# Kernel tuning notes

Measured on AMD Instinct MI355X. Metric: run time of the kernel, lower is better.

The kernel has to match this reference:

```python
import jax, jax.numpy as jnp
import numpy as np

BETA = 0.25
N_E = 8192
E_DIM = 256


def setup_inputs() -> dict:
    key = jax.random.key(0)
    k1, k2 = jax.random.split(key)
    z = jax.random.normal(k1, (16, E_DIM, 32, 32), dtype=jnp.float32)
    # matches torch init: uniform_(-1/n_e, 1/n_e)
    codebook = jax.random.uniform(k2, (N_E, E_DIM), dtype=jnp.float32,
                                  minval=-1.0 / N_E, maxval=1.0 / N_E)
    return {"z": z, "codebook": codebook}


def reference(z, codebook):
    B, C, H, W = z.shape  # C == e_dim
    zp = jnp.transpose(z, (0, 2, 3, 1))          # [B, H, W, C]
    zf = zp.reshape(-1, C)                       # [N, C], N = B*H*W
    # squared L2 distances: ||z||^2 + ||e||^2 - 2 z.e
    d = (jnp.sum(zf * zf, axis=1, keepdims=True)
         + jnp.sum(codebook * codebook, axis=1)
         - 2.0 * jnp.einsum('nc,kc->nk', zf, codebook))  # [N, n_e]
    min_encoding_indices = jnp.argmin(d, axis=1)         # [N]
    z_q = codebook[min_encoding_indices].reshape(zp.shape)  # [B, H, W, C]
    sg = jax.lax.stop_gradient
    loss = jnp.mean((sg(z_q) - zp) ** 2) + BETA * jnp.mean((z_q - sg(zp)) ** 2)
    # straight-through estimator
    z_q_st = zp + sg(z_q - zp)
    z_q_out = jnp.transpose(z_q_st, (0, 3, 1, 2))  # back to NCHW
    return z_q_out, loss, min_encoding_indices
```

## Files before the change

kernel.cpp:

```cpp
#include <hip/hip_runtime.h>

typedef short s8v __attribute__((ext_vector_type(8)));
typedef float f4v __attribute__((ext_vector_type(4)));
typedef float f4 __attribute__((ext_vector_type(4)));
typedef unsigned short u16v4 __attribute__((ext_vector_type(4)));

#define N_PIX 16384
#define NE    8192
#define EDIM  256
#define ZQ_ELEMS 4194304
#define MARGIN 4.5e-4f
#define NGRP 512

__device__ __forceinline__ float bf2f(unsigned short u) {
    union { unsigned int i; float f; } c; c.i = ((unsigned int)u) << 16; return c.f;
}
__device__ __forceinline__ unsigned short f2bf(float f) {
    unsigned int u = __float_as_uint(f);
    u = (u + 0x7fffu + ((u >> 16) & 1u)) >> 16;
    return (unsigned short)u;
}
__device__ __forceinline__ unsigned short f2bf_down(float f) {
    unsigned int u = __float_as_uint(f);
    unsigned short b = (unsigned short)(u >> 16);
    if ((u & 0xFFFFu) && (u >> 31)) b += 1;
    return b;
}

__device__ __forceinline__ float np_pw128sq(const float* a) {
    float r[8];
    #pragma unroll
    for (int j = 0; j < 8; ++j) r[j] = __fmul_rn(a[j], a[j]);
    for (int i = 8; i < 128; i += 8)
        #pragma unroll
        for (int j = 0; j < 8; ++j) r[j] = __fadd_rn(r[j], __fmul_rn(a[i + j], a[i + j]));
    return __fadd_rn(__fadd_rn(__fadd_rn(r[0], r[1]), __fadd_rn(r[2], r[3])),
                     __fadd_rn(__fadd_rn(r[4], r[5]), __fadd_rn(r[6], r[7])));
}


__global__ __launch_bounds__(256) void vq_pre(const float* __restrict__ z,
                                              const float* __restrict__ cb,
                                              unsigned short* __restrict__ z16,
                                              unsigned short* __restrict__ cb16,
                                              float* __restrict__ esum32,
                                              int do_z) {
    __shared__ unsigned short zl[64 * 66];
    int t = threadIdx.x;
    int bx = blockIdx.x;
    if (bx < 1024) {
        if (!do_z) return;
        int p0 = (bx >> 2) * 64;
        int c0 = (bx & 3) * 64;
        int b = p0 >> 10, hw0 = p0 & 1023;
        const float* src = z + (((size_t)b * 256 + c0) << 10) + hw0;
        #pragma unroll
        for (int i = 0; i < 4; ++i) {
            int idx = i * 256 + t;
            int ch = idx >> 4, pq = idx & 15;
            f4 v = *(const f4*)(src + ((size_t)ch << 10) + pq * 4);
            #pragma unroll
            for (int e = 0; e < 4; ++e) zl[(pq * 4 + e) * 66 + ch] = f2bf(v[e]);
        }
        __syncthreads();
        #pragma unroll
        for (int i = 0; i < 2; ++i) {
            int idx = i * 256 + t;
            int px = idx >> 3, cc = idx & 7;
            s8v o;
            #pragma unroll
            for (int e = 0; e < 8; ++e) o[e] = (short)zl[px * 66 + cc * 8 + e];
            *(s8v*)&z16[((size_t)(p0 + px)) * 256 + c0 + cc * 8] = o;
        }
    } else {
        int base = (bx - 1024) * 32;
        const float* src = cb + (size_t)base * EDIM;
        unsigned short* dst = cb16 + (size_t)base * EDIM;
        #pragma unroll
        for (int i = 0; i < 8; ++i) {
            int e0 = (i * 256 + t) * 4;
            f4 v = *(const f4*)(src + e0);
            u16v4 o;
            o.x = f2bf(v[0]); o.y = f2bf(v[1]); o.z = f2bf(v[2]); o.w = f2bf(v[3]);
            *(u16v4*)(dst + e0) = o;
        }
        if (t < 32) {
            const float* a = cb + (size_t)(base + t) * EDIM;
            esum32[base + t] = __fadd_rn(np_pw128sq(a), np_pw128sq(a + 128));
        }
    }
}

__global__ __launch_bounds__(512, 2) void vq_phase1g(const unsigned short* __restrict__ cb16,
                                                     const unsigned short* __restrict__ z16,
                                                     unsigned short* __restrict__ gmin) {
    __shared__ unsigned short L[2][32768];
    const int t = threadIdx.x;
    const int wave = t >> 6, lane = t & 63;
    const int q = lane >> 4, r = lane & 15;
    const int wr = wave >> 2, wc = wave & 3;
    const int cm0 = ((int)blockIdx.x >> 3) * 256;
    const int pg  = (int)blockIdx.x & 7;

    const int pc0 = t, pc1 = t + 512;
    const int row0 = pc0 >> 2, row1 = pc1 >> 2;
    const int lc0 = (pc0 & 3) ^ ((row0 >> 1) & 3);
    const int lc1 = (pc1 & 3) ^ ((row1 >> 1) & 3);
    const int go0 = row0 * 256 + lc0 * 8;
    const int go1 = row1 * 256 + lc1 * 8;
    const int ld0 = pc0 * 8;
    const int ld1 = pc1 * 8;

    const unsigned short* gA = cb16 + (size_t)cm0 * 256;
    const unsigned short* gB0 = z16 + (size_t)pg * 2048 * 256;

    f4v acc[8][4];
    const f4v zz = {0.f, 0.f, 0.f, 0.f};
    #pragma unroll
    for (int mi = 0; mi < 8; ++mi)
        #pragma unroll
        for (int ni = 0; ni < 4; ++ni) acc[mi][ni] = zz;

    const int cxo = (q ^ ((r >> 1) & 3)) * 8;
    const int aro = (wr * 128 + r) * 32 + cxo;
    const int bro = 16384 + (wc * 64 + r) * 32 + cxo;

#define GLL(g, l) __builtin_amdgcn_global_load_lds( \
        (const __attribute__((address_space(1))) unsigned int*)(g), \
        (__attribute__((address_space(3))) unsigned int*)(l), 16, 0, 0)
#define STAGEKT(buf_, gk_, gBp_) do { \
        unsigned short* Lb_ = &L[(buf_)][0]; \
        GLL(gA + go0 + (gk_),            Lb_ + ld0); \
        GLL(gA + go1 + (gk_),            Lb_ + ld1); \
        GLL(gA + go0 + 32 + (gk_),       Lb_ + 8192 + ld0); \
        GLL(gA + go1 + 32 + (gk_),       Lb_ + 8192 + ld1); \
        GLL((gBp_) + go0 + (gk_),        Lb_ + 16384 + ld0); \
        GLL((gBp_) + go1 + (gk_),        Lb_ + 16384 + ld1); \
        GLL((gBp_) + go0 + 32 + (gk_),   Lb_ + 16384 + 8192 + ld0); \
        GLL((gBp_) + go1 + 32 + (gk_),   Lb_ + 16384 + 8192 + ld1); } while (0)
#define ARD(Lp, mi, ks) (*(const s8v*)&(Lp)[(ks) * 8192 + (mi) * 512 + aro])
#define BRD(Lp, ni, ks) (*(const s8v*)&(Lp)[(ks) * 8192 + (ni) * 512 + bro])
#define MFMA16(Aset, Bset, mo) do { \
        __builtin_amdgcn_s_setprio(1); \
        _Pragma("unroll") \
        for (int mi = 0; mi < 4; ++mi) \
            _Pragma("unroll") \
            for (int ni = 0; ni < 4; ++ni) \
                acc[(mo) + mi][ni] = __builtin_amdgcn_mfma_f32_16x16x32_bf16( \
                    Aset[mi], Bset[ni], acc[(mo) + mi][ni], 0, 0, 0); \
        __builtin_amdgcn_s_setprio(0); } while (0)

    STAGEKT(0, 0, gB0);
    asm volatile("s_waitcnt vmcnt(0)" ::: "memory");
    __builtin_amdgcn_s_barrier();

    for (int it = 0; it < 32; ++it) {
        const int buf = it & 1;
        const unsigned short* Lb = &L[buf][0];
        const int nit = it + 1;
        const bool st = nit < 32;

        __builtin_amdgcn_s_barrier();
        if (st) {
            STAGEKT(buf ^ 1, (nit & 3) * 64, gB0 + (size_t)(nit >> 2) * 65536);
            asm volatile("s_waitcnt vmcnt(8)" ::: "memory");
        } else {
            asm volatile("s_waitcnt vmcnt(0)" ::: "memory");
        }
        __builtin_amdgcn_s_barrier();
        __builtin_amdgcn_sched_barrier(0);

        s8v A0[4], A1[4], B0[4], B1[4];
        #pragma unroll
        for (int ni = 0; ni < 4; ++ni) B0[ni] = BRD(Lb, ni, 0);
        #pragma unroll
        for (int mi = 0; mi < 4; ++mi) A0[mi] = ARD(Lb, mi, 0);
        #pragma unroll
        for (int mi = 0; mi < 4; ++mi) A1[mi] = ARD(Lb, 4 + mi, 0);
        __builtin_amdgcn_sched_barrier(0);
        MFMA16(A0, B0, 0);

        #pragma unroll
        for (int mi = 0; mi < 4; ++mi) A0[mi] = ARD(Lb, mi, 1);
        #pragma unroll
        for (int ni = 0; ni < 4; ++ni) B1[ni] = BRD(Lb, ni, 1);
        __builtin_amdgcn_sched_barrier(0);
        MFMA16(A1, B0, 4);

        #pragma unroll
        for (int mi = 0; mi < 4; ++mi) A1[mi] = ARD(Lb, 4 + mi, 1);
        __builtin_amdgcn_sched_barrier(0);
        MFMA16(A0, B1, 0);

        __builtin_amdgcn_sched_barrier(0);
        MFMA16(A1, B1, 4);

        if ((it & 3) == 3) {
            const int pn0 = pg * 2048 + (it >> 2) * 256;
            #pragma unroll
            for (int mi = 0; mi < 8; ++mi) {
                int g = cm0 / 16 + wr * 8 + mi;
                #pragma unroll
                for (int ni = 0; ni < 4; ++ni) {
                    f4v a = acc[mi][ni];
                    float mx = fmaxf(fmaxf(a[0], a[1]), fmaxf(a[2], a[3]));
                    mx = fmaxf(mx, __shfl_xor(mx, 16));
                    mx = fmaxf(mx, __shfl_xor(mx, 32));
                    if (q == 0) {
                        int pxc = (pn0 + wc * 64 + ni * 16) >> 4;
                        gmin[(size_t)pxc * 8192 + g * 16 + r] = f2bf_down(-2.0f * mx);
                    }
                    acc[mi][ni] = zz;
                }
            }
        }
    }
#undef MFMA16
#undef BRD
#undef ARD
#undef STAGEKT
#undef GLL
}

__global__ __launch_bounds__(512, 2) void vq_phase1(const float* __restrict__ z,
                                                    const unsigned short* __restrict__ cb16,
                                                    unsigned short* __restrict__ gmin) {
    const int t = threadIdx.x;
    const int wave = t >> 6, lane = t & 63;
    const int col = lane & 15, q = lane >> 4;
    const int mb = (blockIdx.x >> 1) * 64;
    const int chalf = blockIdx.x & 1;

    s8v Z[4][8];
    #pragma unroll
    for (int pt = 0; pt < 4; ++pt) {
        int n = mb + pt * 16 + col;
        const float* zb = z + ((size_t)(n >> 10) << 18) + (size_t)(n & 1023);
        #pragma unroll
        for (int c0 = 0; c0 < 8; ++c0) {
            s8v a;
            #pragma unroll
            for (int j = 0; j < 8; ++j) {
                int c = c0 * 32 + q * 8 + j;
                a[j] = (short)f2bf(zb[(size_t)c << 10]);
            }
            Z[pt][c0] = a;
        }
    }

    const int kbase = chalf * 4096 + wave * 512;
    for (int it = 0; it < 16; ++it) {
        int n0 = kbase + it * 32;
        const unsigned short* bb = cb16 + (size_t)(n0 + col) * EDIM + q * 8;
        f4v zz = {0.f, 0.f, 0.f, 0.f};
        f4v acc[4][2];
        #pragma unroll
        for (int pt = 0; pt < 4; ++pt) { acc[pt][0] = zz; acc[pt][1] = zz; }
        #pragma unroll
        for (int c0 = 0; c0 < 8; ++c0) {
            s8v C0 = *(const s8v*)(bb + c0 * 32);
            s8v C1 = *(const s8v*)(bb + 16 * EDIM + c0 * 32);
            #pragma unroll
            for (int pt = 0; pt < 4; ++pt) {
                acc[pt][0] = __builtin_amdgcn_mfma_f32_16x16x32_bf16(C0, Z[pt][c0], acc[pt][0], 0, 0, 0);
                acc[pt][1] = __builtin_amdgcn_mfma_f32_16x16x32_bf16(C1, Z[pt][c0], acc[pt][1], 0, 0, 0);
            }
        }
        int gbase = chalf * 256 + wave * 32 + it * 2;
        #pragma unroll
        for (int pt = 0; pt < 4; ++pt) {
            #pragma unroll
            for (int s = 0; s < 2; ++s) {
                f4v a = acc[pt][s];
                float mx = fmaxf(fmaxf(a[0], a[1]), fmaxf(a[2], a[3]));
                mx = fmaxf(mx, __shfl_xor(mx, 16));
                mx = fmaxf(mx, __shfl_xor(mx, 32));
                if (q == 0)
                    gmin[(size_t)((mb >> 4) + pt) * 8192 + (gbase + s) * 16 + col] =
                        f2bf_down(-2.0f * mx);
            }
        }
    }
}

__global__ __launch_bounds__(256) void vq_phase2(const float* __restrict__ z,
                                                 const float* __restrict__ cb,
                                                 const float* __restrict__ esum32,
                                                 const unsigned short* __restrict__ gmin,
                                                 unsigned int* __restrict__ idxw) {
    __shared__ float zt[32 * 260];
    __shared__ unsigned short gm[NGRP * 33];
    __shared__ float zs[32];
    __shared__ int pq;
    int t = threadIdx.x;
    int lane = t & 63;
    int p0 = blockIdx.x * 32;
    int bb = p0 >> 10, inner = p0 & 1023;

    if (t == 0) pq = 0;
    const float* zb = z + (((size_t)bb * 256) << 10) + inner;
    #pragma unroll
    for (int i = 0; i < 8; ++i) {
        int job = i * 256 + t;
        int c = job >> 3, qq = job & 7;
        f4 v = *(const f4*)(zb + ((size_t)c << 10) + qq * 4);
        #pragma unroll
        for (int e = 0; e < 4; ++e) zt[(qq * 4 + e) * 260 + c] = v[e];
    }
    const unsigned short* gsrc = gmin + (size_t)(2 * blockIdx.x) * 8192;
    #pragma unroll
    for (int j = 0; j < 8; ++j) {
        int li8 = (j * 256 + t) * 8;
        s8v v = *(const s8v*)(gsrc + li8);
        int h = li8 >> 13, rem = li8 & 8191;
        int g = rem >> 4, r0 = rem & 15;
        #pragma unroll
        for (int e = 0; e < 8; ++e) gm[g * 33 + h * 16 + r0 + e] = (unsigned short)v[e];
    }
    __syncthreads();
    if (t < 32) {
        const float* a = zt + t * 260;
        zs[t] = __fadd_rn(np_pw128sq(a), np_pw128sq(a + 128));
    }
    __syncthreads();

#define DOT_TAIL(sv) do { sv += __shfl_xor(sv, 1); sv += __shfl_xor(sv, 2); } while (0)
#define MERGE(dv, kv) do { if ((dv) < bd || ((dv) == bd && (kv) < bk)) { bd = (dv); bk = (kv); } } while (0)

    while (true) {
        int p;
        if (lane == 0) p = atomicAdd(&pq, 1);
        p = __shfl(p, 0);
        if (p >= 32) break;

        float lmin = 3.0e38f;
        #pragma unroll
        for (int j = 0; j < 8; ++j) lmin = fminf(lmin, bf2f(gm[(lane * 8 + j) * 33 + p]));
        #pragma unroll
        for (int m = 1; m < 64; m <<= 1) lmin = fminf(lmin, __shfl_xor(lmin, m));
        float thr = lmin + MARGIN;
        float zsp = zs[p];
        const f4* zr = (const f4*)(zt + p * 260) + (lane & 3);

        float bd = 3.0e38f; int bk = 0x7FFFFFFF;
        int pend = -1;
        for (int j = 0; j < 8; ++j) {
            unsigned long long mask = __ballot(bf2f(gm[(lane * 8 + j) * 33 + p]) <= thr);
            while (mask) {
                int lb = __builtin_ctzll(mask); mask &= mask - 1;
                int g = lb * 8 + j;
                if (pend < 0) { pend = g; continue; }
                int k1 = pend * 16 + (lane >> 2), k2 = g * 16 + (lane >> 2);
                const f4* c1 = (const f4*)(cb + (size_t)k1 * EDIM) + (lane & 3);
                const f4* c2 = (const f4*)(cb + (size_t)k2 * EDIM) + (lane & 3);
                double a0 = 0.0, a1 = 0.0, a2 = 0.0, a3 = 0.0;
                double b0 = 0.0, b1 = 0.0, b2 = 0.0, b3 = 0.0;
                #pragma unroll
                for (int i = 0; i < 16; ++i) {
                    f4 x = zr[i * 4], y1 = c1[i * 4], y2 = c2[i * 4];
                    a0 = fma((double)x[0], (double)y1[0], a0);
                    b0 = fma((double)x[0], (double)y2[0], b0);
                    a1 = fma((double)x[1], (double)y1[1], a1);
                    b1 = fma((double)x[1], (double)y2[1], b1);
                    a2 = fma((double)x[2], (double)y1[2], a2);
                    b2 = fma((double)x[2], (double)y2[2], b2);
                    a3 = fma((double)x[3], (double)y1[3], a3);
                    b3 = fma((double)x[3], (double)y2[3], b3);
                }
                double s1 = (a0 + a1) + (a2 + a3);
                double s2 = (b0 + b1) + (b2 + b3);
                DOT_TAIL(s1); DOT_TAIL(s2);
                float E1 = (float)s1, E2 = (float)s2;
                float d1 = __fsub_rn(__fadd_rn(zsp, esum32[k1]), __fmul_rn(2.0f, E1));
                float d2 = __fsub_rn(__fadd_rn(zsp, esum32[k2]), __fmul_rn(2.0f, E2));
                MERGE(d1, k1); MERGE(d2, k2);
                pend = -1;
            }
        }
        if (pend >= 0) {
            int k = pend * 16 + (lane >> 2);
            const f4* cr = (const f4*)(cb + (size_t)k * EDIM) + (lane & 3);
            double a0 = 0.0, a1 = 0.0, a2 = 0.0, a3 = 0.0;
            #pragma unroll
            for (int i = 0; i < 16; ++i) {
                f4 x = zr[i * 4], y = cr[i * 4];
                a0 = fma((double)x[0], (double)y[0], a0);
                a1 = fma((double)x[1], (double)y[1], a1);
                a2 = fma((double)x[2], (double)y[2], a2);
                a3 = fma((double)x[3], (double)y[3], a3);
            }
            double s = (a0 + a1) + (a2 + a3);
            DOT_TAIL(s);
            float E = (float)s;
            float d = __fsub_rn(__fadd_rn(zsp, esum32[k]), __fmul_rn(2.0f, E));
            MERGE(d, k);
        }
        #pragma unroll
        for (int m = 1; m < 64; m <<= 1) {
            float od = __shfl_xor(bd, m); int ok = __shfl_xor(bk, m);
            if (od < bd || (od == bd && ok < bk)) { bd = od; bk = ok; }
        }
        if (lane == 0) idxw[p0 + p] = (unsigned int)bk;
    }
#undef MERGE
#undef DOT_TAIL
}

__global__ __launch_bounds__(256) void vq_emit(const float* __restrict__ cb,
                                               const float* __restrict__ z,
                                               const unsigned int* __restrict__ idxw,
                                               float* __restrict__ outf,
                                               float* __restrict__ lossw) {
    __shared__ float qrow[1024 * 17];
    __shared__ unsigned int lidx[1024];
    __shared__ float red[4];
    int t = threadIdx.x;
    int gtid = blockIdx.x * 256 + t;
    if (gtid < N_PIX) outf[ZQ_ELEMS + 1 + gtid] = (float)(idxw[gtid] & (NE - 1));

    int b = blockIdx.x >> 4;
    int c0 = (blockIdx.x & 15) * 16;

    #pragma unroll
    for (int j = 0; j < 4; ++j)
        lidx[j * 256 + t] = idxw[b * 1024 + j * 256 + t] & (NE - 1);
    __syncthreads();
    #pragma unroll
    for (int j = 0; j < 16; ++j) {
        int p = j * 64 + (t >> 2);
        f4 v = *(const f4*)(cb + (size_t)lidx[p] * EDIM + c0 + (t & 3) * 4);
        #pragma unroll
        for (int e = 0; e < 4; ++e) qrow[p * 17 + (t & 3) * 4 + e] = v[e];
    }
    __syncthreads();

    float acc = 0.f;
    size_t base = (size_t)blockIdx.x * 16384;
    for (int i = 0; i < 64; ++i) {
        size_t o = base + (size_t)i * 256 + t;
        int c = (int)((o >> 10) & 255);
        int p = (int)(o & 1023);
        float qv = qrow[p * 17 + (c - c0)];
        outf[o] = qv;
        float d = qv - z[o];
        acc = fmaf(d, d, acc);
    }
    #pragma unroll
    for (int off = 32; off > 0; off >>= 1) acc += __shfl_down(acc, off);
    if ((t & 63) == 0) red[t >> 6] = acc;
    __syncthreads();
    if (t == 0) atomicAdd(lossw, red[0] + red[1] + red[2] + red[3]);
}

__global__ void vq_finalize(const float* __restrict__ lossw, float* __restrict__ loss_out) {
    loss_out[0] = 1.25f * lossw[0] * (1.0f / 4194304.0f);
}

extern "C" void kernel_launch(void* const* d_in, const int* in_sizes, int n_in,
                              void* d_out, int out_size, void* d_ws, size_t ws_size,
                              hipStream_t stream) {
    const float* z  = (const float*)d_in[0];
    const float* cb = (const float*)d_in[1];
    float* outf = (float*)d_out;
    unsigned short* gmin = (unsigned short*)d_out;

    char* w = (char*)d_ws;
    unsigned short* cb16   = (unsigned short*)w;
    float*          esum32 = (float*)(w + 4194304);
    unsigned int*   idxw   = (unsigned int*)(w + 4227072);
    float*          lossw  = (float*)(w + 4292608);
    unsigned short* z16    = (unsigned short*)(w + 4292864);

    if (ws_size < 4292864) return;
    const bool big_ws = (ws_size >= 12681472);

    hipMemsetAsync(lossw, 0, sizeof(float), stream);
    vq_pre<<<1280, 256, 0, stream>>>(z, cb, z16, cb16, esum32, big_ws ? 1 : 0);
    if (big_ws) {
        vq_phase1g<<<(NE / 256) * (N_PIX / 2048), 512, 0, stream>>>(cb16, z16, gmin);
    } else {
        vq_phase1 <<<(N_PIX / 64) * 2, 512, 0, stream>>>(z, cb16, gmin);
    }
    vq_phase2  <<<N_PIX / 32, 256, 0, stream>>>(z, cb, esum32, gmin, idxw);
    vq_emit    <<<256, 256, 0, stream>>>(cb, z, idxw, outf, lossw);
    vq_finalize<<<1, 1, 0, stream>>>(lossw, outf + ZQ_ELEMS);
}
```

Baseline: 246.9 us.

## Prefetch next-tile fragments in GEMM loop; fold loss into phase2 and drop finalize

The phase1g main loop now issues the next tile's global-to-LDS staging early, waits on it mid-iteration, and preloads the first A/B register fragments for the next iteration before the last MFMA block. This overlaps LDS reads with MFMA work and removes one barrier from the loop head. The loss is now computed in phase2 from the chosen codebook row and the cached z, accumulated into 64 partial slots. vq_emit therefore stops re-reading z, writes with vectorized stores, and folds the finalize kernel into its first block. The tradeoffs are higher register pressure in the GEMM, a full vmcnt(0) wait inside the loop, and extra atomics in phase2.

```diff
diff --git a/kernel.cpp b/kernel.cpp
--- a/kernel.cpp
+++ b/kernel.cpp
@@ -153,28 +153,22 @@
     STAGEKT(0, 0, gB0);
     asm volatile("s_waitcnt vmcnt(0)" ::: "memory");
     __builtin_amdgcn_s_barrier();
+    s8v A0[4], A1[4], B0[4], B1[4];
+    #pragma unroll
+    for (int ni = 0; ni < 4; ++ni) B0[ni] = BRD(&L[0][0], ni, 0);
+    #pragma unroll
+    for (int mi = 0; mi < 4; ++mi) A0[mi] = ARD(&L[0][0], mi, 0);
 
     for (int it = 0; it < 32; ++it) {
         const int buf = it & 1;
         const unsigned short* Lb = &L[buf][0];
+        const unsigned short* Ln = &L[buf ^ 1][0];
         const int nit = it + 1;
         const bool st = nit < 32;
 
         __builtin_amdgcn_s_barrier();
-        if (st) {
-            STAGEKT(buf ^ 1, (nit & 3) * 64, gB0 + (size_t)(nit >> 2) * 65536);
-            asm volatile("s_waitcnt vmcnt(8)" ::: "memory");
-        } else {
-            asm volatile("s_waitcnt vmcnt(0)" ::: "memory");
-        }
-        __builtin_amdgcn_s_barrier();
-        __builtin_amdgcn_sched_barrier(0);
-
-        s8v A0[4], A1[4], B0[4], B1[4];
-        #pragma unroll
-        for (int ni = 0; ni < 4; ++ni) B0[ni] = BRD(Lb, ni, 0);
-        #pragma unroll
-        for (int mi = 0; mi < 4; ++mi) A0[mi] = ARD(Lb, mi, 0);
+        if (st) STAGEKT(buf ^ 1, (nit & 3) * 64, gB0 + (size_t)(nit >> 2) * 65536);
+
         #pragma unroll
         for (int mi = 0; mi < 4; ++mi) A1[mi] = ARD(Lb, 4 + mi, 0);
         __builtin_amdgcn_sched_barrier(0);
@@ -192,6 +186,14 @@
         __builtin_amdgcn_sched_barrier(0);
         MFMA16(A0, B1, 0);
 
+        if (st) {
+            asm volatile("s_waitcnt vmcnt(0)" ::: "memory");
+            __builtin_amdgcn_s_barrier();
+            #pragma unroll
+            for (int ni = 0; ni < 4; ++ni) B0[ni] = BRD(Ln, ni, 0);
+            #pragma unroll
+            for (int mi = 0; mi < 4; ++mi) A0[mi] = ARD(Ln, mi, 0);
+        }
         __builtin_amdgcn_sched_barrier(0);
         MFMA16(A1, B1, 4);
 
@@ -287,13 +289,14 @@
                                                  const float* __restrict__ cb,
                                                  const float* __restrict__ esum32,
                                                  const unsigned short* __restrict__ gmin,
-                                                 unsigned int* __restrict__ idxw) {
+                                                 unsigned int* __restrict__ idxw,
+                                                 float* __restrict__ lossparts) {
     __shared__ float zt[32 * 260];
     __shared__ unsigned short gm[NGRP * 33];
     __shared__ float zs[32];
     __shared__ int pq;
     int t = threadIdx.x;
-    int lane = t & 63;
+    int wave = t >> 6, lane = t & 63;
     int p0 = blockIdx.x * 32;
     int bb = p0 >> 10, inner = p0 & 1023;
 
@@ -327,6 +330,7 @@
 #define DOT_TAIL(sv) do { sv += __shfl_xor(sv, 1); sv += __shfl_xor(sv, 2); } while (0)
 #define MERGE(dv, kv) do { if ((dv) < bd || ((dv) == bd && (kv) < bk)) { bd = (dv); bk = (kv); } } while (0)
 
+    float wls = 0.f;
     while (true) {
         int p;
         if (lane == 0) p = atomicAdd(&pq, 1);
@@ -401,22 +405,39 @@
             if (od < bd || (od == bd && ok < bk)) { bd = od; bk = ok; }
         }
         if (lane == 0) idxw[p0 + p] = (unsigned int)bk;
-    }
+
+        float s0 = 0.f;
+        #pragma unroll
+        for (int e = 0; e < 4; ++e) {
+            float cv = cb[(size_t)bk * EDIM + lane + 64 * e];
+            float zv = zt[p * 260 + lane + 64 * e];
+            float dx = cv - zv; s0 = fmaf(dx, dx, s0);
+        }
+        wls += s0;
+    }
+    #pragma unroll
+    for (int m = 1; m < 64; m <<= 1) wls += __shfl_xor(wls, m);
+    if (lane == 0)
+        atomicAdd(&lossparts[(((int)blockIdx.x << 2) + wave) & 63], wls);
 #undef MERGE
 #undef DOT_TAIL
 }
 
 __global__ __launch_bounds__(256) void vq_emit(const float* __restrict__ cb,
-                                               const float* __restrict__ z,
                                                const unsigned int* __restrict__ idxw,
-                                               float* __restrict__ outf,
-                                               float* __restrict__ lossw) {
+                                               const float* __restrict__ lossparts,
+                                               float* __restrict__ outf) {
     __shared__ float qrow[1024 * 17];
     __shared__ unsigned int lidx[1024];
-    __shared__ float red[4];
     int t = threadIdx.x;
     int gtid = blockIdx.x * 256 + t;
     if (gtid < N_PIX) outf[ZQ_ELEMS + 1 + gtid] = (float)(idxw[gtid] & (NE - 1));
+    if (blockIdx.x == 0 && t < 64) {
+        double v = (double)lossparts[t];
+        #pragma unroll
+        for (int m = 1; m < 64; m <<= 1) v += __shfl_xor(v, m);
+        if (t == 0) outf[ZQ_ELEMS] = 1.25f * (float)(v * (1.0 / 4194304.0));
+    }
 
     int b = blockIdx.x >> 4;
     int c0 = (blockIdx.x & 15) * 16;
@@ -434,26 +455,14 @@
     }
     __syncthreads();
 
-    float acc = 0.f;
     size_t base = (size_t)blockIdx.x * 16384;
-    for (int i = 0; i < 64; ++i) {
-        size_t o = base + (size_t)i * 256 + t;
-        int c = (int)((o >> 10) & 255);
-        int p = (int)(o & 1023);
-        float qv = qrow[p * 17 + (c - c0)];
-        outf[o] = qv;
-        float d = qv - z[o];
-        acc = fmaf(d, d, acc);
-    }
-    #pragma unroll
-    for (int off = 32; off > 0; off >>= 1) acc += __shfl_down(acc, off);
-    if ((t & 63) == 0) red[t >> 6] = acc;
-    __syncthreads();
-    if (t == 0) atomicAdd(lossw, red[0] + red[1] + red[2] + red[3]);
-}
-
-__global__ void vq_finalize(const float* __restrict__ lossw, float* __restrict__ loss_out) {
-    loss_out[0] = 1.25f * lossw[0] * (1.0f / 4194304.0f);
+    #pragma unroll
+    for (int i = 0; i < 16; ++i) {
+        f4 v;
+        #pragma unroll
+        for (int e = 0; e < 4; ++e) v[e] = qrow[(t * 4 + e) * 17 + i];
+        *(f4*)&outf[base + (size_t)i * 1024 + t * 4] = v;
+    }
 }
 
 extern "C" void kernel_launch(void* const* d_in, const int* in_sizes, int n_in,
@@ -465,23 +474,22 @@
     unsigned short* gmin = (unsigned short*)d_out;
 
     char* w = (char*)d_ws;
-    unsigned short* cb16   = (unsigned short*)w;
-    float*          esum32 = (float*)(w + 4194304);
-    unsigned int*   idxw   = (unsigned int*)(w + 4227072);
-    float*          lossw  = (float*)(w + 4292608);
-    unsigned short* z16    = (unsigned short*)(w + 4292864);
+    unsigned short* cb16     = (unsigned short*)w;
+    float*          esum32   = (float*)(w + 4194304);
+    unsigned int*   idxw     = (unsigned int*)(w + 4227072);
+    float*          lossparts= (float*)(w + 4292608);
+    unsigned short* z16      = (unsigned short*)(w + 4292864);
 
     if (ws_size < 4292864) return;
     const bool big_ws = (ws_size >= 12681472);
 
-    hipMemsetAsync(lossw, 0, sizeof(float), stream);
+    hipMemsetAsync(lossparts, 0, 256, stream);
     vq_pre<<<1280, 256, 0, stream>>>(z, cb, z16, cb16, esum32, big_ws ? 1 : 0);
     if (big_ws) {
         vq_phase1g<<<(NE / 256) * (N_PIX / 2048), 512, 0, stream>>>(cb16, z16, gmin);
     } else {
         vq_phase1 <<<(N_PIX / 64) * 2, 512, 0, stream>>>(z, cb16, gmin);
     }
-    vq_phase2  <<<N_PIX / 32, 256, 0, stream>>>(z, cb, esum32, gmin, idxw);
-    vq_emit    <<<256, 256, 0, stream>>>(cb, z, idxw, outf, lossw);
-    vq_finalize<<<1, 1, 0, stream>>>(lossw, outf + ZQ_ELEMS);
-}
+    vq_phase2  <<<N_PIX / 32, 256, 0, stream>>>(z, cb, esum32, gmin, idxw, lossparts);
+    vq_emit    <<<256, 256, 0, stream>>>(cb, idxw, lossparts, outf);
+}
```

Measured after the change: 236.4 us. 1.04x faster.
